# Kernel optimization log

Measured on AMD Instinct MI355X. Metric: run time of the kernel, lower is better.

Reference implementation:

```python
import jax, jax.numpy as jnp
import numpy as np

B, S, D, KC = 32, 4096, 64, 256  # batch*heads, seq_len, head_dim, compressed dim


def setup_inputs() -> dict:
    key = jax.random.key(0)
    ks = jax.random.split(key, 7)
    return {
        "Q": jax.random.normal(ks[0], (B, S, D), dtype=jnp.float32),
        "K": jax.random.normal(ks[1], (B, S, D), dtype=jnp.float32),
        "V": jax.random.normal(ks[2], (B, S, D), dtype=jnp.float32),
        "E_w": jax.random.normal(ks[3], (KC, S), dtype=jnp.float32) * (1.0 / np.sqrt(S)),
        "E_b": jax.random.normal(ks[4], (KC,), dtype=jnp.float32) * 0.01,
        "F_w": jax.random.normal(ks[5], (KC, S), dtype=jnp.float32) * (1.0 / np.sqrt(S)),
        "F_b": jax.random.normal(ks[6], (KC,), dtype=jnp.float32) * 0.01,
    }


def reference(Q, K, V, E_w, E_b, F_w, F_b):
    # K: [B,S,D] -> transpose -> [B,D,S]; E proj over seq axis -> [B,D,KC]
    Ke = jnp.einsum("bsd,ks->bdk", K, E_w) + E_b  # [B, D, KC]
    # scores: Q @ E(K) -> [B, S, KC], scaled by sqrt(head_dim)
    scale = jnp.sqrt(jnp.asarray(D, dtype=Q.dtype))
    P = jnp.einsum("bsd,bdk->bsk", Q, Ke) / scale
    # causal mask: torch.triu(ones(S, KC)) keeps (i, j) where j >= i
    i = jnp.arange(S)[:, None]
    j = jnp.arange(KC)[None, :]
    keep = j >= i  # [S, KC]
    P = jnp.where(keep[None, :, :], P, jnp.asarray(-1e10, dtype=P.dtype))
    P = jax.nn.softmax(P, axis=-1)  # dropout p=0.0 -> identity
    # V: [B,S,D] -> [B,D,S]; F proj -> [B,D,KC]; transpose -> [B,KC,D]
    Vf = jnp.einsum("bsd,ks->bkd", V, F_w) + F_b[None, :, None]  # [B, KC, D]
    out = jnp.einsum("bsk,bkd->bsd", P, Vf)  # [B, S, D]
    return out
```

## Files before the change

### kernel.cpp

```cpp
#include <hip/hip_runtime.h>
#include <hip/hip_bf16.h>
#include <math.h>

#define NB  32
#define NS  4096
#define ND  64
#define NKC 256
#define ASTR 72
#define PSTR 260
#define PBSTR 264

typedef __attribute__((ext_vector_type(8))) short short8;
typedef __attribute__((ext_vector_type(4))) short sv4;
typedef __attribute__((ext_vector_type(4))) float f32x4;

__device__ __forceinline__ short f2bf(float f) {
    union { float f; unsigned u; } v; v.f = f;
    return (short)((v.u + 0x7FFFu + ((v.u >> 16) & 1u)) >> 16);
}
__device__ __forceinline__ float bf2f(short s) {
    union { unsigned u; float f; } v;
    v.u = ((unsigned)(unsigned short)s) << 16; return v.f;
}

__global__ __launch_bounds__(256) void proj_gemm(
    const float* __restrict__ Ew, const float* __restrict__ Fw,
    const float* __restrict__ K,  const float* __restrict__ V,
    float* __restrict__ KeT, float* __restrict__ Vf)
{
    const int b     = blockIdx.x;
    const int chunk = blockIdx.y;
    const int z     = blockIdx.z;
    const int mt = z >> 1, mm = z & 1;
    const float* __restrict__ A  = mm ? Fw : Ew;
    const float* __restrict__ Bg = mm ? V  : K;
    float* __restrict__ Cout     = mm ? Vf : KeT;

    const int t = threadIdx.x, wave = t >> 6, lane = t & 63;
    const int lm = lane & 15, g = lane >> 4;
    __shared__ short As[64 * ASTR];
    __shared__ short Bs[64 * ASTR];
    const int k0 = mt * 64;
    const size_t bBase = (size_t)b * NS * ND;
    const int rowA = t >> 4, qA = t & 15;
    const int dB = t & 31, sB = t >> 5;

    f32x4 acc[4];
#pragma unroll
    for (int i = 0; i < 4; ++i) acc[i] = (f32x4){0.f, 0.f, 0.f, 0.f};

    const int sBeg = chunk * 512, sEnd = sBeg + 512;
    float4 pa[4];
    float2 pb[8];
#pragma unroll
    for (int i = 0; i < 4; ++i)
        pa[i] = *(const float4*)&A[(size_t)(k0 + i * 16 + rowA) * NS + sBeg + qA * 4];
#pragma unroll
    for (int i = 0; i < 8; ++i)
        pb[i] = *(const float2*)&Bg[bBase + (size_t)(sBeg + sB * 8 + i) * ND + dB * 2];

    for (int s0 = sBeg; s0 < sEnd; s0 += 64) {
#pragma unroll
        for (int i = 0; i < 4; ++i) {
            sv4 sv;
            sv.x = f2bf(pa[i].x); sv.y = f2bf(pa[i].y);
            sv.z = f2bf(pa[i].z); sv.w = f2bf(pa[i].w);
            *(sv4*)&As[(i * 16 + rowA) * ASTR + qA * 4] = sv;
        }
        {
            short8 w0, w1;
#pragma unroll
            for (int i = 0; i < 8; ++i) { w0[i] = f2bf(pb[i].x); w1[i] = f2bf(pb[i].y); }
            *(short8*)&Bs[(dB * 2 + 0) * ASTR + sB * 8] = w0;
            *(short8*)&Bs[(dB * 2 + 1) * ASTR + sB * 8] = w1;
        }
        __syncthreads();
        if (s0 + 64 < sEnd) {
#pragma unroll
            for (int i = 0; i < 4; ++i)
                pa[i] = *(const float4*)&A[(size_t)(k0 + i * 16 + rowA) * NS + s0 + 64 + qA * 4];
#pragma unroll
            for (int i = 0; i < 8; ++i)
                pb[i] = *(const float2*)&Bg[bBase + (size_t)(s0 + 64 + sB * 8 + i) * ND + dB * 2];
        }
#pragma unroll
        for (int ks = 0; ks < 64; ks += 32) {
            short8 a = *(const short8*)&As[(wave * 16 + lm) * ASTR + ks + g * 8];
#pragma unroll
            for (int nt = 0; nt < 4; ++nt) {
                short8 bb = *(const short8*)&Bs[(nt * 16 + lm) * ASTR + ks + g * 8];
                acc[nt] = __builtin_amdgcn_mfma_f32_16x16x32_bf16(a, bb, acc[nt], 0, 0, 0);
            }
        }
        __syncthreads();
    }
#pragma unroll
    for (int r = 0; r < 4; ++r) {
        int kc = k0 + wave * 16 + g * 4 + r;
#pragma unroll
        for (int nt = 0; nt < 4; ++nt)
            atomicAdd(&Cout[((size_t)b * NKC + kc) * ND + nt * 16 + lm], acc[nt][r]);
    }
}

__global__ __launch_bounds__(256) void convert_bias(
    const float* __restrict__ KeT, const float* __restrict__ Vf,
    const float* __restrict__ Eb,  const float* __restrict__ Fb,
    short* __restrict__ KeTb, short* __restrict__ VfTb)
{
    const int b = blockIdx.y, kt = blockIdx.x, t = threadIdx.x;
    const int kk = t >> 4, dq = t & 15;
    const int k = kt * 16 + kk;
    __shared__ short Ls[16][68];

    const size_t off = ((size_t)b * NKC + k) * ND + dq * 4;

    float4 a = *(const float4*)&KeT[off];
    float eb = Eb[k];
    sv4 w;
    w.x = f2bf(a.x + eb); w.y = f2bf(a.y + eb);
    w.z = f2bf(a.z + eb); w.w = f2bf(a.w + eb);
    *(sv4*)&KeTb[off] = w;

    float4 v = *(const float4*)&Vf[off];
    float fb = Fb[k];
    sv4 u;
    u.x = f2bf(v.x + fb); u.y = f2bf(v.y + fb);
    u.z = f2bf(v.z + fb); u.w = f2bf(v.w + fb);
    *(sv4*)&Ls[kk][dq * 4] = u;
    __syncthreads();

    const int d = t >> 2, ks = t & 3;
    sv4 o;
    o.x = Ls[ks * 4 + 0][d]; o.y = Ls[ks * 4 + 1][d];
    o.z = Ls[ks * 4 + 2][d]; o.w = Ls[ks * 4 + 3][d];
    *(sv4*)&VfTb[((size_t)b * ND + d) * NKC + kt * 16 + ks * 4] = o;
}

__global__ __launch_bounds__(256) void attn_fused(
    const float* __restrict__ Q, const short* __restrict__ KeTb,
    const short* __restrict__ VfTb, float* __restrict__ out)
{
    const int x = blockIdx.x, b = blockIdx.y, t = threadIdx.x;

    if (x >= 8) {
        const int ch = x - 8;
        __shared__ float part[4][65];
        __shared__ float mv[64];
        const int d = t >> 2, seg = t & 3;
        const short* vp = &VfTb[((size_t)b * ND + d) * NKC + seg * 64];
        float s = 0.f;
#pragma unroll
        for (int i = 0; i < 8; ++i) {
            short8 h = *(const short8*)&vp[i * 8];
#pragma unroll
            for (int j = 0; j < 8; ++j) s += bf2f(h[j]);
        }
        part[seg][d] = s;
        __syncthreads();
        if (t < 64)
            mv[t] = (part[0][t] + part[1][t] + part[2][t] + part[3][t]) * (1.f / 256.f);
        __syncthreads();
#pragma unroll
        for (int i = 0; i < 15; ++i) {
            int idx = i * 256 + t, row = idx >> 4, q = idx & 15;
            *(float4*)&out[((size_t)b * NS + 256 + ch * 240 + row) * ND + q * 4] =
                *(const float4*)&mv[q * 4];
        }
        return;
    }

    const int s0 = x * 32;
    const int wave = t >> 6, lane = t & 63, lm = lane & 15, g = lane >> 4;
    __shared__ short Qs[32 * ASTR];
    __shared__ float Ps[32 * PSTR];
    __shared__ short PsB[32 * PBSTR];

    {
        int row = t >> 3, dq = t & 7;
        size_t off = ((size_t)b * NS + s0 + row) * ND + dq * 8;
        float4 q0 = *(const float4*)&Q[off], q1 = *(const float4*)&Q[off + 4];
        short8 w;
        w[0] = f2bf(q0.x); w[1] = f2bf(q0.y); w[2] = f2bf(q0.z); w[3] = f2bf(q0.w);
        w[4] = f2bf(q1.x); w[5] = f2bf(q1.y); w[6] = f2bf(q1.z); w[7] = f2bf(q1.w);
        *(short8*)&Qs[row * ASTR + dq * 8] = w;
    }
    __syncthreads();

    const int rt = wave & 1, kh = wave >> 1;
#pragma unroll
    for (int kk = 0; kk < 8; ++kk) {
        int kt = kh * 8 + kk;
        f32x4 acc = (f32x4){0.f, 0.f, 0.f, 0.f};
#pragma unroll
        for (int ks = 0; ks < 64; ks += 32) {
            short8 a  = *(const short8*)&Qs[(rt * 16 + lm) * ASTR + ks + g * 8];
            short8 bb = *(const short8*)&KeTb[((size_t)b * NKC + kt * 16 + lm) * ND + ks + g * 8];
            acc = __builtin_amdgcn_mfma_f32_16x16x32_bf16(a, bb, acc, 0, 0, 0);
        }
        int col = kt * 16 + lm;
#pragma unroll
        for (int r = 0; r < 4; ++r) {
            int rowg = s0 + rt * 16 + g * 4 + r;
            Ps[(rt * 16 + g * 4 + r) * PSTR + col] =
                (col >= rowg) ? acc[r] * 0.125f : -1e30f;
        }
    }
    __syncthreads();

    for (int rr = wave * 8; rr < wave * 8 + 8; ++rr) {
        float v0 = Ps[rr * PSTR + lane],       v1 = Ps[rr * PSTR + lane + 64];
        float v2 = Ps[rr * PSTR + lane + 128], v3 = Ps[rr * PSTR + lane + 192];
        float m = fmaxf(fmaxf(v0, v1), fmaxf(v2, v3));
        for (int off = 32; off; off >>= 1) m = fmaxf(m, __shfl_xor(m, off, 64));
        float e0 = __expf(v0 - m), e1 = __expf(v1 - m);
        float e2 = __expf(v2 - m), e3 = __expf(v3 - m);
        float s = e0 + e1 + e2 + e3;
        for (int off = 32; off; off >>= 1) s += __shfl_xor(s, off, 64);
        float inv = 1.f / s;
        PsB[rr * PBSTR + lane]       = f2bf(e0 * inv);
        PsB[rr * PBSTR + lane + 64]  = f2bf(e1 * inv);
        PsB[rr * PBSTR + lane + 128] = f2bf(e2 * inv);
        PsB[rr * PBSTR + lane + 192] = f2bf(e3 * inv);
    }
    __syncthreads();

    const int dt = wave;
    f32x4 oa[2];
    oa[0] = (f32x4){0.f, 0.f, 0.f, 0.f};
    oa[1] = (f32x4){0.f, 0.f, 0.f, 0.f};
    for (int ks = x; ks < 8; ++ks) {
        short8 bb = *(const short8*)&VfTb[((size_t)b * ND + dt * 16 + lm) * NKC + ks * 32 + g * 8];
#pragma unroll
        for (int r2 = 0; r2 < 2; ++r2) {
            short8 a = *(const short8*)&PsB[(r2 * 16 + lm) * PBSTR + ks * 32 + g * 8];
            oa[r2] = __builtin_amdgcn_mfma_f32_16x16x32_bf16(a, bb, oa[r2], 0, 0, 0);
        }
    }
#pragma unroll
    for (int r2 = 0; r2 < 2; ++r2)
#pragma unroll
        for (int r = 0; r < 4; ++r)
            out[((size_t)b * NS + s0 + r2 * 16 + g * 4 + r) * ND + dt * 16 + lm] = oa[r2][r];
}

extern "C" void kernel_launch(void* const* d_in, const int* in_sizes, int n_in,
                              void* d_out, int out_size, void* d_ws, size_t ws_size,
                              hipStream_t stream) {
    (void)in_sizes; (void)n_in; (void)out_size; (void)ws_size;
    const float* Q  = (const float*)d_in[0];
    const float* K  = (const float*)d_in[1];
    const float* V  = (const float*)d_in[2];
    const float* Ew = (const float*)d_in[3];
    const float* Eb = (const float*)d_in[4];
    const float* Fw = (const float*)d_in[5];
    const float* Fb = (const float*)d_in[6];
    float* out = (float*)d_out;

    const size_t nKe = (size_t)NB * NKC * ND;
    float* KeT  = (float*)d_ws;
    float* Vf   = KeT + nKe;
    short* KeTb = (short*)(Vf + nKe);
    short* VfTb = KeTb + nKe;

    hipMemsetAsync(d_ws, 0, 2 * nKe * sizeof(float), stream);
    proj_gemm<<<dim3(NB, 8, 8), 256, 0, stream>>>(Ew, Fw, K, V, KeT, Vf);
    convert_bias<<<dim3(16, NB), 256, 0, stream>>>(KeT, Vf, Eb, Fb, KeTb, VfTb);
    attn_fused<<<dim3(24, NB), 256, 0, stream>>>(Q, KeTb, VfTb, out);
}
```

Baseline: 191.1 us.

## Restructure projection GEMM and fuse bias/convert into attention kernel

The projection GEMM now has each block compute all 256 compressed rows for one 512-row sequence chunk. This reuses each staged K/V tile across four M tiles and cuts the redundant K/V reads, at the cost of more registers and LDS. A prep kernel converts E_w/F_w to bf16 once and zeroes the workspace, replacing the memset, when the workspace is large enough. The separate convert_bias kernel is removed: bias add, bf16 conversion and the V transpose now happen inside the attention kernel. The softmax drops the max subtraction and computes exponentials in registers with a cross-wave sum reduction, and the mean-fill region is spread over more blocks.

```diff
diff --git a/kernel.cpp b/kernel.cpp
--- a/kernel.cpp
+++ b/kernel.cpp
@@ -7,65 +7,92 @@
 #define ND  64
 #define NKC 256
 #define ASTR 72
-#define PSTR 260
 #define PBSTR 264
+#define VSTR  264
 
 typedef __attribute__((ext_vector_type(8))) short short8;
-typedef __attribute__((ext_vector_type(4))) short sv4;
 typedef __attribute__((ext_vector_type(4))) float f32x4;
 
 __device__ __forceinline__ short f2bf(float f) {
     union { float f; unsigned u; } v; v.f = f;
     return (short)((v.u + 0x7FFFu + ((v.u >> 16) & 1u)) >> 16);
 }
-__device__ __forceinline__ float bf2f(short s) {
-    union { unsigned u; float f; } v;
-    v.u = ((unsigned)(unsigned short)s) << 16; return v.f;
-}
-
+
+__global__ __launch_bounds__(256) void prep(
+    const float* __restrict__ Ew, const float* __restrict__ Fw,
+    float4* __restrict__ zws, short* __restrict__ EwB, short* __restrict__ FwB)
+{
+    const int gid = blockIdx.x * 256 + threadIdx.x;
+    zws[gid] = (float4){0.f, 0.f, 0.f, 0.f};
+
+    const int half = (NKC * NS) / 8;
+    const float* src = (gid < half) ? Ew : Fw;
+    short* dst       = (gid < half) ? EwB : FwB;
+    const int i8 = (gid < half) ? gid : gid - half;
+    float4 a = *(const float4*)&src[(size_t)i8 * 8];
+    float4 c = *(const float4*)&src[(size_t)i8 * 8 + 4];
+    short8 w;
+    w[0] = f2bf(a.x); w[1] = f2bf(a.y); w[2] = f2bf(a.z); w[3] = f2bf(a.w);
+    w[4] = f2bf(c.x); w[5] = f2bf(c.y); w[6] = f2bf(c.z); w[7] = f2bf(c.w);
+    *(short8*)&dst[(size_t)i8 * 8] = w;
+}
+
+template <typename AT>
 __global__ __launch_bounds__(256) void proj_gemm(
-    const float* __restrict__ Ew, const float* __restrict__ Fw,
-    const float* __restrict__ K,  const float* __restrict__ V,
+    const AT* __restrict__ EwX, const AT* __restrict__ FwX,
+    const float* __restrict__ K, const float* __restrict__ V,
     float* __restrict__ KeT, float* __restrict__ Vf)
 {
-    const int b     = blockIdx.x;
-    const int chunk = blockIdx.y;
-    const int z     = blockIdx.z;
-    const int mt = z >> 1, mm = z & 1;
-    const float* __restrict__ A  = mm ? Fw : Ew;
-    const float* __restrict__ Bg = mm ? V  : K;
-    float* __restrict__ Cout     = mm ? Vf : KeT;
+    const int x = blockIdx.x, b = blockIdx.y;
+    const int chunk = x >> 1, mm = x & 1;
+    const AT* __restrict__ Ab    = mm ? FwX : EwX;
+    const float* __restrict__ Bg = mm ? V   : K;
+    float* __restrict__ Cout     = mm ? Vf  : KeT;
 
     const int t = threadIdx.x, wave = t >> 6, lane = t & 63;
     const int lm = lane & 15, g = lane >> 4;
-    __shared__ short As[64 * ASTR];
+    __shared__ short As[256 * ASTR];
     __shared__ short Bs[64 * ASTR];
-    const int k0 = mt * 64;
     const size_t bBase = (size_t)b * NS * ND;
-    const int rowA = t >> 4, qA = t & 15;
+    const int rA = t >> 3, jA = t & 7;
     const int dB = t & 31, sB = t >> 5;
 
-    f32x4 acc[4];
-#pragma unroll
-    for (int i = 0; i < 4; ++i) acc[i] = (f32x4){0.f, 0.f, 0.f, 0.f};
+    f32x4 acc[4][4];
+#pragma unroll
+    for (int mt = 0; mt < 4; ++mt)
+#pragma unroll
+        for (int nt = 0; nt < 4; ++nt) acc[mt][nt] = (f32x4){0.f, 0.f, 0.f, 0.f};
 
     const int sBeg = chunk * 512, sEnd = sBeg + 512;
-    float4 pa[4];
+    short8 pa[8];
+    float4 paf[16];
     float2 pb[8];
 #pragma unroll
-    for (int i = 0; i < 4; ++i)
-        pa[i] = *(const float4*)&A[(size_t)(k0 + i * 16 + rowA) * NS + sBeg + qA * 4];
+    for (int i = 0; i < 8; ++i) {
+        if constexpr (sizeof(AT) == 2) {
+            pa[i] = *(const short8*)&Ab[(size_t)(i * 32 + rA) * NS + sBeg + jA * 8];
+        } else {
+            paf[2 * i]     = *(const float4*)&Ab[(size_t)(i * 32 + rA) * NS + sBeg + jA * 8];
+            paf[2 * i + 1] = *(const float4*)&Ab[(size_t)(i * 32 + rA) * NS + sBeg + jA * 8 + 4];
+        }
+    }
 #pragma unroll
     for (int i = 0; i < 8; ++i)
         pb[i] = *(const float2*)&Bg[bBase + (size_t)(sBeg + sB * 8 + i) * ND + dB * 2];
 
     for (int s0 = sBeg; s0 < sEnd; s0 += 64) {
 #pragma unroll
-        for (int i = 0; i < 4; ++i) {
-            sv4 sv;
-            sv.x = f2bf(pa[i].x); sv.y = f2bf(pa[i].y);
-            sv.z = f2bf(pa[i].z); sv.w = f2bf(pa[i].w);
-            *(sv4*)&As[(i * 16 + rowA) * ASTR + qA * 4] = sv;
+        for (int i = 0; i < 8; ++i) {
+            if constexpr (sizeof(AT) == 2) {
+                *(short8*)&As[(i * 32 + rA) * ASTR + jA * 8] = pa[i];
+            } else {
+                short8 w;
+                w[0] = f2bf(paf[2 * i].x);     w[1] = f2bf(paf[2 * i].y);
+                w[2] = f2bf(paf[2 * i].z);     w[3] = f2bf(paf[2 * i].w);
+                w[4] = f2bf(paf[2 * i + 1].x); w[5] = f2bf(paf[2 * i + 1].y);
+                w[6] = f2bf(paf[2 * i + 1].z); w[7] = f2bf(paf[2 * i + 1].w);
+                *(short8*)&As[(i * 32 + rA) * ASTR + jA * 8] = w;
+            }
         }
         {
             short8 w0, w1;
@@ -77,94 +104,77 @@
         __syncthreads();
         if (s0 + 64 < sEnd) {
 #pragma unroll
-            for (int i = 0; i < 4; ++i)
-                pa[i] = *(const float4*)&A[(size_t)(k0 + i * 16 + rowA) * NS + s0 + 64 + qA * 4];
+            for (int i = 0; i < 8; ++i) {
+                if constexpr (sizeof(AT) == 2) {
+                    pa[i] = *(const short8*)&Ab[(size_t)(i * 32 + rA) * NS + s0 + 64 + jA * 8];
+                } else {
+                    paf[2 * i]     = *(const float4*)&Ab[(size_t)(i * 32 + rA) * NS + s0 + 64 + jA * 8];
+                    paf[2 * i + 1] = *(const float4*)&Ab[(size_t)(i * 32 + rA) * NS + s0 + 64 + jA * 8 + 4];
+                }
+            }
 #pragma unroll
             for (int i = 0; i < 8; ++i)
                 pb[i] = *(const float2*)&Bg[bBase + (size_t)(s0 + 64 + sB * 8 + i) * ND + dB * 2];
         }
 #pragma unroll
         for (int ks = 0; ks < 64; ks += 32) {
-            short8 a = *(const short8*)&As[(wave * 16 + lm) * ASTR + ks + g * 8];
+            short8 aF[4];
+#pragma unroll
+            for (int mt = 0; mt < 4; ++mt)
+                aF[mt] = *(const short8*)&As[(mt * 64 + wave * 16 + lm) * ASTR + ks + g * 8];
 #pragma unroll
             for (int nt = 0; nt < 4; ++nt) {
-                short8 bb = *(const short8*)&Bs[(nt * 16 + lm) * ASTR + ks + g * 8];
-                acc[nt] = __builtin_amdgcn_mfma_f32_16x16x32_bf16(a, bb, acc[nt], 0, 0, 0);
+                short8 bF = *(const short8*)&Bs[(nt * 16 + lm) * ASTR + ks + g * 8];
+#pragma unroll
+                for (int mt = 0; mt < 4; ++mt)
+                    acc[mt][nt] = __builtin_amdgcn_mfma_f32_16x16x32_bf16(aF[mt], bF, acc[mt][nt], 0, 0, 0);
             }
         }
         __syncthreads();
     }
 #pragma unroll
-    for (int r = 0; r < 4; ++r) {
-        int kc = k0 + wave * 16 + g * 4 + r;
-#pragma unroll
-        for (int nt = 0; nt < 4; ++nt)
-            atomicAdd(&Cout[((size_t)b * NKC + kc) * ND + nt * 16 + lm], acc[nt][r]);
-    }
-}
-
-__global__ __launch_bounds__(256) void convert_bias(
-    const float* __restrict__ KeT, const float* __restrict__ Vf,
-    const float* __restrict__ Eb,  const float* __restrict__ Fb,
-    short* __restrict__ KeTb, short* __restrict__ VfTb)
-{
-    const int b = blockIdx.y, kt = blockIdx.x, t = threadIdx.x;
-    const int kk = t >> 4, dq = t & 15;
-    const int k = kt * 16 + kk;
-    __shared__ short Ls[16][68];
-
-    const size_t off = ((size_t)b * NKC + k) * ND + dq * 4;
-
-    float4 a = *(const float4*)&KeT[off];
-    float eb = Eb[k];
-    sv4 w;
-    w.x = f2bf(a.x + eb); w.y = f2bf(a.y + eb);
-    w.z = f2bf(a.z + eb); w.w = f2bf(a.w + eb);
-    *(sv4*)&KeTb[off] = w;
-
-    float4 v = *(const float4*)&Vf[off];
-    float fb = Fb[k];
-    sv4 u;
-    u.x = f2bf(v.x + fb); u.y = f2bf(v.y + fb);
-    u.z = f2bf(v.z + fb); u.w = f2bf(v.w + fb);
-    *(sv4*)&Ls[kk][dq * 4] = u;
-    __syncthreads();
-
-    const int d = t >> 2, ks = t & 3;
-    sv4 o;
-    o.x = Ls[ks * 4 + 0][d]; o.y = Ls[ks * 4 + 1][d];
-    o.z = Ls[ks * 4 + 2][d]; o.w = Ls[ks * 4 + 3][d];
-    *(sv4*)&VfTb[((size_t)b * ND + d) * NKC + kt * 16 + ks * 4] = o;
+    for (int mt = 0; mt < 4; ++mt)
+#pragma unroll
+        for (int r = 0; r < 4; ++r) {
+            int kc = mt * 64 + wave * 16 + g * 4 + r;
+#pragma unroll
+            for (int nt = 0; nt < 4; ++nt)
+                atomicAdd(&Cout[((size_t)b * NKC + kc) * ND + nt * 16 + lm], acc[mt][nt][r]);
+        }
 }
 
 __global__ __launch_bounds__(256) void attn_fused(
-    const float* __restrict__ Q, const short* __restrict__ KeTb,
-    const short* __restrict__ VfTb, float* __restrict__ out)
+    const float* __restrict__ Q,  const float* __restrict__ KeT,
+    const float* __restrict__ Vf, const float* __restrict__ Eb,
+    const float* __restrict__ Fb, float* __restrict__ out)
 {
     const int x = blockIdx.x, b = blockIdx.y, t = threadIdx.x;
 
     if (x >= 8) {
-        const int ch = x - 8;
-        __shared__ float part[4][65];
+        __shared__ float pq[16][64];
         __shared__ float mv[64];
-        const int d = t >> 2, seg = t & 3;
-        const short* vp = &VfTb[((size_t)b * ND + d) * NKC + seg * 64];
-        float s = 0.f;
-#pragma unroll
-        for (int i = 0; i < 8; ++i) {
-            short8 h = *(const short8*)&vp[i * 8];
-#pragma unroll
-            for (int j = 0; j < 8; ++j) s += bf2f(h[j]);
-        }
-        part[seg][d] = s;
+        const int kg = t >> 4, dq = t & 15;
+        float4 s4 = (float4){0.f, 0.f, 0.f, 0.f};
+        for (int p = 0; p < 16; ++p) {
+            int k = p * 16 + kg;
+            float4 v = *(const float4*)&Vf[((size_t)b * NKC + k) * ND + dq * 4];
+            float fb = Fb[k];
+            s4.x += v.x + fb; s4.y += v.y + fb; s4.z += v.z + fb; s4.w += v.w + fb;
+        }
+        *(float4*)&pq[kg][dq * 4] = s4;
         __syncthreads();
-        if (t < 64)
-            mv[t] = (part[0][t] + part[1][t] + part[2][t] + part[3][t]) * (1.f / 256.f);
+        if (t < 64) {
+            float m = 0.f;
+#pragma unroll
+            for (int i = 0; i < 16; ++i) m += pq[i][t];
+            mv[t] = m * (1.f / 256.f);
+        }
         __syncthreads();
-#pragma unroll
-        for (int i = 0; i < 15; ++i) {
+        const int r0 = 256 + (x - 8) * 64;
+#pragma unroll
+        for (int i = 0; i < 4; ++i) {
             int idx = i * 256 + t, row = idx >> 4, q = idx & 15;
-            *(float4*)&out[((size_t)b * NS + 256 + ch * 240 + row) * ND + q * 4] =
+            *(float4*)&out[((size_t)b * NS + r0 + row) * ND + q * 4] =
                 *(const float4*)&mv[q * 4];
         }
         return;
@@ -173,8 +183,9 @@
     const int s0 = x * 32;
     const int wave = t >> 6, lane = t & 63, lm = lane & 15, g = lane >> 4;
     __shared__ short Qs[32 * ASTR];
-    __shared__ float Ps[32 * PSTR];
     __shared__ short PsB[32 * PBSTR];
+    __shared__ short VfT[64 * VSTR];
+    __shared__ float rsums[32][4];
 
     {
         int row = t >> 3, dq = t & 7;
@@ -185,69 +196,107 @@
         w[4] = f2bf(q1.x); w[5] = f2bf(q1.y); w[6] = f2bf(q1.z); w[7] = f2bf(q1.w);
         *(short8*)&Qs[row * ASTR + dq * 8] = w;
     }
+    {
+        const int dB = t & 31, sB = t >> 5;
+#pragma unroll
+        for (int pass = 0; pass < 4; ++pass) {
+            int kb = pass * 64 + sB * 8;
+            float2 v[8]; float fb[8];
+#pragma unroll
+            for (int i = 0; i < 8; ++i) {
+                v[i]  = *(const float2*)&Vf[((size_t)b * NKC + kb + i) * ND + dB * 2];
+                fb[i] = Fb[kb + i];
+            }
+            short8 w0, w1;
+#pragma unroll
+            for (int i = 0; i < 8; ++i) {
+                w0[i] = f2bf(v[i].x + fb[i]);
+                w1[i] = f2bf(v[i].y + fb[i]);
+            }
+            *(short8*)&VfT[(dB * 2 + 0) * VSTR + kb] = w0;
+            *(short8*)&VfT[(dB * 2 + 1) * VSTR + kb] = w1;
+        }
+    }
     __syncthreads();
 
-    const int rt = wave & 1, kh = wave >> 1;
-#pragma unroll
-    for (int kk = 0; kk < 8; ++kk) {
-        int kt = kh * 8 + kk;
-        f32x4 acc = (f32x4){0.f, 0.f, 0.f, 0.f};
-#pragma unroll
-        for (int ks = 0; ks < 64; ks += 32) {
-            short8 a  = *(const short8*)&Qs[(rt * 16 + lm) * ASTR + ks + g * 8];
-            short8 bb = *(const short8*)&KeTb[((size_t)b * NKC + kt * 16 + lm) * ND + ks + g * 8];
-            acc = __builtin_amdgcn_mfma_f32_16x16x32_bf16(a, bb, acc, 0, 0, 0);
-        }
-        int col = kt * 16 + lm;
+    f32x4 accP[2][4];
+#pragma unroll
+    for (int rt = 0; rt < 2; ++rt)
+#pragma unroll
+        for (int kk = 0; kk < 4; ++kk) accP[rt][kk] = (f32x4){0.f, 0.f, 0.f, 0.f};
+#pragma unroll
+    for (int kk = 0; kk < 4; ++kk) {
+        int kt = wave * 4 + kk;
+        float ebv = Eb[kt * 16 + lm];
+#pragma unroll
+        for (int ks2 = 0; ks2 < 2; ++ks2) {
+            const float* kp = &KeT[((size_t)b * NKC + kt * 16 + lm) * ND + ks2 * 32 + g * 8];
+            float4 c0 = *(const float4*)kp, c1 = *(const float4*)(kp + 4);
+            short8 bf;
+            bf[0] = f2bf(c0.x + ebv); bf[1] = f2bf(c0.y + ebv);
+            bf[2] = f2bf(c0.z + ebv); bf[3] = f2bf(c0.w + ebv);
+            bf[4] = f2bf(c1.x + ebv); bf[5] = f2bf(c1.y + ebv);
+            bf[6] = f2bf(c1.z + ebv); bf[7] = f2bf(c1.w + ebv);
+#pragma unroll
+            for (int rt = 0; rt < 2; ++rt) {
+                short8 aq = *(const short8*)&Qs[(rt * 16 + lm) * ASTR + ks2 * 32 + g * 8];
+                accP[rt][kk] = __builtin_amdgcn_mfma_f32_16x16x32_bf16(aq, bf, accP[rt][kk], 0, 0, 0);
+            }
+        }
+    }
+#pragma unroll
+    for (int rt = 0; rt < 2; ++rt)
 #pragma unroll
         for (int r = 0; r < 4; ++r) {
+            float s = 0.f;
             int rowg = s0 + rt * 16 + g * 4 + r;
-            Ps[(rt * 16 + g * 4 + r) * PSTR + col] =
-                (col >= rowg) ? acc[r] * 0.125f : -1e30f;
-        }
-    }
+#pragma unroll
+            for (int kk = 0; kk < 4; ++kk) {
+                int col = wave * 64 + kk * 16 + lm;
+                float e = (col >= rowg) ? __expf(accP[rt][kk][r] * 0.125f) : 0.f;
+                accP[rt][kk][r] = e;
+                s += e;
+            }
+#pragma unroll
+            for (int off = 1; off <= 8; off <<= 1) s += __shfl_xor(s, off, 64);
+            if (lm == 0) rsums[rt * 16 + g * 4 + r][wave] = s;
+        }
     __syncthreads();
-
-    for (int rr = wave * 8; rr < wave * 8 + 8; ++rr) {
-        float v0 = Ps[rr * PSTR + lane],       v1 = Ps[rr * PSTR + lane + 64];
-        float v2 = Ps[rr * PSTR + lane + 128], v3 = Ps[rr * PSTR + lane + 192];
-        float m = fmaxf(fmaxf(v0, v1), fmaxf(v2, v3));
-        for (int off = 32; off; off >>= 1) m = fmaxf(m, __shfl_xor(m, off, 64));
-        float e0 = __expf(v0 - m), e1 = __expf(v1 - m);
-        float e2 = __expf(v2 - m), e3 = __expf(v3 - m);
-        float s = e0 + e1 + e2 + e3;
-        for (int off = 32; off; off >>= 1) s += __shfl_xor(s, off, 64);
-        float inv = 1.f / s;
-        PsB[rr * PBSTR + lane]       = f2bf(e0 * inv);
-        PsB[rr * PBSTR + lane + 64]  = f2bf(e1 * inv);
-        PsB[rr * PBSTR + lane + 128] = f2bf(e2 * inv);
-        PsB[rr * PBSTR + lane + 192] = f2bf(e3 * inv);
-    }
+#pragma unroll
+    for (int rt = 0; rt < 2; ++rt)
+#pragma unroll
+        for (int r = 0; r < 4; ++r) {
+            float4 rs = *(const float4*)&rsums[rt * 16 + g * 4 + r][0];
+            float inv = 1.f / (rs.x + rs.y + rs.z + rs.w);
+#pragma unroll
+            for (int kk = 0; kk < 4; ++kk)
+                PsB[(rt * 16 + g * 4 + r) * PBSTR + wave * 64 + kk * 16 + lm] =
+                    f2bf(accP[rt][kk][r] * inv);
+        }
     __syncthreads();
 
-    const int dt = wave;
     f32x4 oa[2];
     oa[0] = (f32x4){0.f, 0.f, 0.f, 0.f};
     oa[1] = (f32x4){0.f, 0.f, 0.f, 0.f};
     for (int ks = x; ks < 8; ++ks) {
-        short8 bb = *(const short8*)&VfTb[((size_t)b * ND + dt * 16 + lm) * NKC + ks * 32 + g * 8];
-#pragma unroll
-        for (int r2 = 0; r2 < 2; ++r2) {
-            short8 a = *(const short8*)&PsB[(r2 * 16 + lm) * PBSTR + ks * 32 + g * 8];
-            oa[r2] = __builtin_amdgcn_mfma_f32_16x16x32_bf16(a, bb, oa[r2], 0, 0, 0);
-        }
-    }
-#pragma unroll
-    for (int r2 = 0; r2 < 2; ++r2)
+        short8 bv = *(const short8*)&VfT[(wave * 16 + lm) * VSTR + ks * 32 + g * 8];
+#pragma unroll
+        for (int rt = 0; rt < 2; ++rt) {
+            short8 av = *(const short8*)&PsB[(rt * 16 + lm) * PBSTR + ks * 32 + g * 8];
+            oa[rt] = __builtin_amdgcn_mfma_f32_16x16x32_bf16(av, bv, oa[rt], 0, 0, 0);
+        }
+    }
+#pragma unroll
+    for (int rt = 0; rt < 2; ++rt)
 #pragma unroll
         for (int r = 0; r < 4; ++r)
-            out[((size_t)b * NS + s0 + r2 * 16 + g * 4 + r) * ND + dt * 16 + lm] = oa[r2][r];
+            out[((size_t)b * NS + s0 + rt * 16 + g * 4 + r) * ND + wave * 16 + lm] = oa[rt][r];
 }
 
 extern "C" void kernel_launch(void* const* d_in, const int* in_sizes, int n_in,
                               void* d_out, int out_size, void* d_ws, size_t ws_size,
                               hipStream_t stream) {
-    (void)in_sizes; (void)n_in; (void)out_size; (void)ws_size;
+    (void)in_sizes; (void)n_in; (void)out_size;
     const float* Q  = (const float*)d_in[0];
     const float* K  = (const float*)d_in[1];
     const float* V  = (const float*)d_in[2];
@@ -258,13 +307,17 @@
     float* out = (float*)d_out;
 
     const size_t nKe = (size_t)NB * NKC * ND;
-    float* KeT  = (float*)d_ws;
-    float* Vf   = KeT + nKe;
-    short* KeTb = (short*)(Vf + nKe);
-    short* VfTb = KeTb + nKe;
-
-    hipMemsetAsync(d_ws, 0, 2 * nKe * sizeof(float), stream);
-    proj_gemm<<<dim3(NB, 8, 8), 256, 0, stream>>>(Ew, Fw, K, V, KeT, Vf);
-    convert_bias<<<dim3(16, NB), 256, 0, stream>>>(KeT, Vf, Eb, Fb, KeTb, VfTb);
-    attn_fused<<<dim3(24, NB), 256, 0, stream>>>(Q, KeTb, VfTb, out);
-}
+    float* KeT = (float*)d_ws;
+    float* Vf  = KeT + nKe;
+
+    if (ws_size >= 8u * 1024 * 1024) {
+        short* EwB = (short*)(Vf + nKe);
+        short* FwB = EwB + (size_t)NKC * NS;
+        prep<<<dim3(1024), 256, 0, stream>>>(Ew, Fw, (float4*)d_ws, EwB, FwB);
+        proj_gemm<short><<<dim3(16, NB), 256, 0, stream>>>(EwB, FwB, K, V, KeT, Vf);
+    } else {
+        hipMemsetAsync(d_ws, 0, 2 * nKe * sizeof(float), stream);
+        proj_gemm<float><<<dim3(16, NB), 256, 0, stream>>>(Ew, Fw, K, V, KeT, Vf);
+    }
+    attn_fused<<<dim3(68, NB), 256, 0, stream>>>(Q, KeT, Vf, Eb, Fb, out);
+}
```

After: 179.3 us. 6.2% less time.
